# Kernel optimization log

Hardware: AMD Instinct MI355X
Metric: run time of the kernel (lower is better)

The kernel has to match this reference:

```python
import jax, jax.numpy as jnp
import numpy as np

B, D, N, MSRC, H = 4, 256, 2048, 2048, 4
DIM = D // H  # per-head dim = 64
EPS = 1e-3


def _conv1x1(W, b, z):
    # 1x1 Conv1d == per-position linear: W [out,in], z [B,in,N]
    return jnp.einsum('oc,bcn->bon', W, z) + b[None, :, None]


def setup_inputs() -> dict:
    key = jax.random.key(0)
    ks = jax.random.split(key, 20)
    s = 0.05
    x = jax.random.normal(ks[0], (B, D, N), dtype=jnp.float32)
    source = jax.random.normal(ks[1], (B, D, MSRC), dtype=jnp.float32)
    mask = (jax.random.uniform(ks[2], (B, N, MSRC)) > 0.3).astype(jnp.float32)
    Wq = jax.random.normal(ks[3], (D, D), jnp.float32) * s
    bq = jax.random.normal(ks[4], (D,), jnp.float32) * s
    Wk = jax.random.normal(ks[5], (D, D), jnp.float32) * s
    bk = jax.random.normal(ks[6], (D,), jnp.float32) * s
    Wv = jax.random.normal(ks[7], (D, D), jnp.float32) * s
    bv = jax.random.normal(ks[8], (D,), jnp.float32) * s
    Wm = jax.random.normal(ks[9], (D, D), jnp.float32) * s
    bm = jax.random.normal(ks[10], (D,), jnp.float32) * s
    W1 = jax.random.normal(ks[11], (2 * D, 2 * D), jnp.float32) * s
    b1 = jax.random.normal(ks[12], (2 * D,), jnp.float32) * s
    gamma = jnp.ones((2 * D,), jnp.float32)
    beta = jnp.zeros((2 * D,), jnp.float32)
    rmean = jax.random.normal(ks[13], (2 * D,), jnp.float32) * 0.1
    rvar = jax.random.uniform(ks[14], (2 * D,), jnp.float32) + 0.5
    W2 = jax.random.normal(ks[15], (D, 2 * D), jnp.float32) * s
    b2 = jnp.zeros((D,), jnp.float32)  # nn.init.constant_(mlp[-1].bias, 0.0)
    return dict(x=x, source=source, mask=mask, Wq=Wq, bq=bq, Wk=Wk, bk=bk,
                Wv=Wv, bv=bv, Wm=Wm, bm=bm, W1=W1, b1=b1, gamma=gamma,
                beta=beta, rmean=rmean, rvar=rvar, W2=W2, b2=b2)


def reference(x, source, mask, Wq, bq, Wk, bk, Wv, bv, Wm, bm,
              W1, b1, gamma, beta, rmean, rvar, W2, b2):
    b = x.shape[0]
    # channel dim split as (dim, heads) per torch .view(B, dim, H, -1)
    q = _conv1x1(Wq, bq, x).reshape(b, DIM, H, -1)        # [B,d,H,N]
    k = _conv1x1(Wk, bk, source).reshape(b, DIM, H, -1)   # [B,d,H,M]
    v = _conv1x1(Wv, bv, source).reshape(b, DIM, H, -1)   # [B,d,H,M]
    scores = jnp.einsum('bdhn,bdhm->bhnm', q, k) / (DIM ** 0.5)
    neg = -jnp.finfo(scores.dtype).max
    scores = jnp.where(mask[:, None, :, :] > 0, scores, neg)
    prob = jax.nn.softmax(scores, axis=-1)                # [B,H,N,M]
    msg = jnp.einsum('bhnm,bdhm->bdhn', prob, v).reshape(b, D, -1)
    message = _conv1x1(Wm, bm, msg)                       # [B,D,N]
    y = jnp.concatenate([x, message], axis=1)             # [B,2D,N]
    h = _conv1x1(W1, b1, y)
    # BatchNorm1d (eval mode, eps=1e-3)
    h = (h - rmean[None, :, None]) * jax.lax.rsqrt(rvar + EPS)[None, :, None]
    h = h * gamma[None, :, None] + beta[None, :, None]
    h = jax.nn.relu(h)
    return _conv1x1(W2, b2, h)                            # [B,D,N]
```

## Files before the change

### kernel.cpp

```cpp
#include <hip/hip_runtime.h>

constexpr int Bb = 4;
constexpr int Dd = 256;
constexpr int Nn = 2048;
constexpr int Mm = 2048;
constexpr int Hh = 4;
constexpr int D2 = 512;
constexpr int NT = Bb * Nn;

#define FMAXV 3.402823466e38f

typedef _Float16 half8 __attribute__((ext_vector_type(8)));
typedef _Float16 half4v __attribute__((ext_vector_type(4)));
typedef _Float16 half2v __attribute__((ext_vector_type(2)));
typedef float f32x4 __attribute__((ext_vector_type(4)));

typedef const __attribute__((address_space(1))) void* gas_p;
typedef __attribute__((address_space(3))) void* las_p;

__device__ __forceinline__ void gload16(const void* g, void* l) {
    __builtin_amdgcn_global_load_lds((gas_p)g, (las_p)l, 16, 0, 0);
}

__global__ __launch_bounds__(256)
void prep_all_kernel(const float* __restrict__ Wq, const float* __restrict__ bq,
                     const float* __restrict__ Wk, const float* __restrict__ bk,
                     const float* __restrict__ Wv, const float* __restrict__ bv,
                     const float* __restrict__ Wm,
                     const float* __restrict__ W1, const float* __restrict__ b1,
                     const float* __restrict__ gamma, const float* __restrict__ beta,
                     const float* __restrict__ rmean, const float* __restrict__ rvar,
                     const float* __restrict__ W2, const float* __restrict__ mask,
                     const float* __restrict__ x, const float* __restrict__ source,
                     _Float16* __restrict__ Wqp, float* __restrict__ bqp,
                     _Float16* __restrict__ Wkvp, float* __restrict__ bkvp,
                     _Float16* __restrict__ Wmp,
                     _Float16* __restrict__ W1p, float* __restrict__ b1f,
                     _Float16* __restrict__ W2p,
                     unsigned long long* __restrict__ bmask,
                     _Float16* __restrict__ Yp, _Float16* __restrict__ Sp) {
    const int r = blockIdx.x, t = threadIdx.x;
    if (r < 256) {
        const int h = r >> 6, d = r & 63, so = d * Hh + h;
        Wqp[r * 256 + t] = (_Float16)Wq[so * 256 + t];
        if (t == 0) bqp[r] = bq[so];
    } else if (r < 768) {
        const int rr = r - 256, part = rr >> 8, o = rr & 255;
        const int h = o >> 6, d = o & 63, so = d * Hh + h;
        const float* Ws = part ? Wv : Wk;
        const float* bs = part ? bv : bk;
        Wkvp[rr * 256 + t] = (_Float16)Ws[so * 256 + t];
        if (t == 0) bkvp[rr] = bs[so];
    } else if (r < 1024) {
        const int o = r - 768;
        const int h = t >> 6, d = t & 63, sk = d * Hh + h;
        Wmp[o * 256 + t] = (_Float16)Wm[o * 256 + sk];
    } else if (r < 1536) {
        const int o = r - 1024;
        const float s = gamma[o] * rsqrtf(rvar[o] + 1e-3f);
        W1p[o * 512 + t]       = (_Float16)(W1[o * 512 + t] * s);
        W1p[o * 512 + t + 256] = (_Float16)(W1[o * 512 + t + 256] * s);
        if (t == 0) b1f[o] = (b1[o] - rmean[o]) * s + beta[o];
    } else if (r < 1792) {
        const int o = r - 1536;
        W2p[o * 512 + t]       = (_Float16)W2[o * 512 + t];
        W2p[o * 512 + t + 256] = (_Float16)W2[o * 512 + t + 256];
    } else if (r < 3840) {
        const int id = r - 1792;
        const int w = t >> 6, lane = t & 63;
        const int row = id * 4 + w;
        const float* mrow = mask + (size_t)row * Mm;
        unsigned long long* brow = bmask + (size_t)row * (Mm / 64);
        #pragma unroll 4
        for (int word = 0; word < Mm / 64; ++word) {
            const float v = mrow[word * 64 + lane];
            const unsigned long long bits = __ballot(v > 0.f);
            if (lane == 0) brow[word] = bits;
        }
    } else {
        __shared__ _Float16 Ts[64][72];
        const int px = r - 3840;
        const int n0 = (px & 31) * 64, c0 = ((px >> 5) & 3) * 64;
        const int z = px >> 7, b = z >> 1, which = z & 1;
        const float* src = which ? source : x;
        _Float16* dst = which ? Sp : Yp;
        const int stride = which ? 256 : 512;
        const int cl = t >> 2, np = (t & 3) * 16;
        const float* sp = src + ((size_t)b * Dd + c0 + cl) * Nn + n0 + np;
        #pragma unroll
        for (int i = 0; i < 4; ++i) {
            float4 v = *(const float4*)(sp + i * 4);
            Ts[np + i * 4 + 0][cl] = (_Float16)v.x;
            Ts[np + i * 4 + 1][cl] = (_Float16)v.y;
            Ts[np + i * 4 + 2][cl] = (_Float16)v.z;
            Ts[np + i * 4 + 3][cl] = (_Float16)v.w;
        }
        __syncthreads();
        const int nl = t >> 2, cp = (t & 3) * 16;
        half8 a0 = *(const half8*)&Ts[nl][cp];
        half8 a1 = *(const half8*)&Ts[nl][cp + 8];
        _Float16* dp = dst + ((size_t)b * Nn + n0 + nl) * stride + c0 + cp;
        *(half8*)dp = a0;
        *(half8*)(dp + 8) = a1;
    }
}

__global__ __launch_bounds__(256)
void gemm4w_kernel(const _Float16* __restrict__ A, const _Float16* __restrict__ A2,
                   const _Float16* __restrict__ W, const float* __restrict__ bias,
                   _Float16* __restrict__ dst0, _Float16* __restrict__ dst1,
                   _Float16* __restrict__ dst2, float* __restrict__ dstF,
                   int K, int sA, int sOut, int modeSel, int relu, float oscale) {
    __shared__ __align__(16) _Float16 As[2 * 128 * 64];
    __shared__ __align__(16) _Float16 Bs[2 * 64 * 64];

    const int t = threadIdx.x;
    const int w = t >> 6, lane = t & 63, quad = lane >> 4, l16 = lane & 15;
    const int n0 = blockIdx.x * 128;
    const int og0 = blockIdx.y * 64;

    int mode = 0, oloc0 = og0;
    const _Float16* Ab = A;
    int sAl = sA;
    _Float16* d0 = dst0;
    float osc = oscale;
    if (modeSel == 3) {
        const int part = blockIdx.y >> 2;
        if (part == 1)      { Ab = A2; sAl = 256; d0 = dst1; oloc0 = og0 - 256; osc = 1.0f; }
        else if (part == 2) { Ab = A2; sAl = 256; mode = 1; oloc0 = og0 - 512; osc = 1.0f; }
    } else if (modeSel == 2) {
        mode = 2;
    }

    const int srow = t >> 3, sslot = t & 7;
    const int schunk = sslot ^ (srow & 7);

    f32x4 acc[2][4] = {};
    const int nk = K / 64;
    int buf = 0;

    {
        #pragma unroll
        for (int c = 0; c < 4; ++c)
            gload16(Ab + (size_t)(n0 + c * 32 + srow) * sAl + schunk * 8,
                    As + c * 2048 + t * 8);
        #pragma unroll
        for (int c = 0; c < 2; ++c)
            gload16(W + (size_t)(og0 + c * 32 + srow) * K + schunk * 8,
                    Bs + c * 2048 + t * 8);
        __asm__ volatile("s_waitcnt vmcnt(0)" ::: "memory");
        __syncthreads();
    }

    #pragma unroll 1
    for (int kt = 0; kt < nk; ++kt) {
        if (kt + 1 < nk) {
            const int k0 = (kt + 1) * 64, nb = buf ^ 1;
            #pragma unroll
            for (int c = 0; c < 4; ++c)
                gload16(Ab + (size_t)(n0 + c * 32 + srow) * sAl + k0 + schunk * 8,
                        As + nb * 8192 + c * 2048 + t * 8);
            #pragma unroll
            for (int c = 0; c < 2; ++c)
                gload16(W + (size_t)(og0 + c * 32 + srow) * K + k0 + schunk * 8,
                        Bs + nb * 4096 + c * 2048 + t * 8);
        }
        #pragma unroll
        for (int ks = 0; ks < 2; ++ks) {
            const int csw = ((ks * 4 + quad) ^ (l16 & 7)) * 8;
            half8 af[2], bf[4];
            #pragma unroll
            for (int i = 0; i < 2; ++i)
                af[i] = *(const half8*)&As[buf * 8192 + (w * 32 + i * 16 + l16) * 64 + csw];
            #pragma unroll
            for (int j = 0; j < 4; ++j)
                bf[j] = *(const half8*)&Bs[buf * 4096 + (j * 16 + l16) * 64 + csw];
            #pragma unroll
            for (int i = 0; i < 2; ++i)
                #pragma unroll
                for (int j = 0; j < 4; ++j)
                    acc[i][j] = __builtin_amdgcn_mfma_f32_16x16x32_f16(af[i], bf[j], acc[i][j], 0, 0, 0);
        }
        if (kt + 1 < nk) {
            __asm__ volatile("s_waitcnt vmcnt(0)" ::: "memory");
            __syncthreads();
            buf ^= 1;
        }
    }

    float bcol[4];
    #pragma unroll
    for (int j = 0; j < 4; ++j) bcol[j] = bias[og0 + j * 16 + l16];

    if (mode == 0) {
        _Float16* Escr = As + w * 2048;
        #pragma unroll
        for (int i = 0; i < 2; ++i) {
            #pragma unroll
            for (int j = 0; j < 4; ++j)
                #pragma unroll
                for (int reg = 0; reg < 4; ++reg) {
                    float v = (acc[i][j][reg] + bcol[j]) * osc;
                    if (relu) v = fmaxf(v, 0.f);
                    Escr[(quad * 4 + reg) * 72 + j * 16 + l16] = (_Float16)v;
                }
            __asm__ volatile("s_waitcnt lgkmcnt(0)" ::: "memory");
            const int row = lane & 15, oseg = (lane >> 4) * 16;
            half8 e0 = *(const half8*)&Escr[row * 72 + oseg];
            half8 e1 = *(const half8*)&Escr[row * 72 + oseg + 8];
            _Float16* dp = d0 + (size_t)(n0 + w * 32 + i * 16 + row) * sOut + oloc0 + oseg;
            *(half8*)dp = e0;
            *(half8*)(dp + 8) = e1;
            __asm__ volatile("s_waitcnt lgkmcnt(0)" ::: "memory");
        }
    } else if (mode == 1) {
        #pragma unroll
        for (int i = 0; i < 2; ++i)
            #pragma unroll
            for (int j = 0; j < 4; ++j) {
                const int c = j * 16 + l16;
                const int mloc = w * 32 + i * 16 + quad * 4;
                const int sw = l16 * 8;
                half4v pv;
                #pragma unroll
                for (int reg = 0; reg < 4; ++reg)
                    pv[reg] = (_Float16)(acc[i][j][reg] + bcol[j]);
                *(half4v*)&As[c * 128 + (mloc ^ sw)] = pv;
            }
        __syncthreads();
        const int n0m = n0 & 2047, bidx = n0 >> 11;
        #pragma unroll
        for (int r = 0; r < 2; ++r) {
            const int c = (t >> 3) + r * 32;
            const int mch = (t & 7) * 16;
            const int sw = (c & 15) * 8;
            half8 v0 = *(const half8*)&As[c * 128 + (mch ^ sw)];
            half8 v1 = *(const half8*)&As[c * 128 + ((mch + 8) ^ sw)];
            _Float16* dp = dst2 + ((size_t)bidx * 256 + oloc0 + c) * (size_t)Mm + n0m + mch;
            *(half8*)dp = v0;
            *(half8*)(dp + 8) = v1;
        }
    } else {
        __syncthreads();
        float* scr = (float*)As;
        #pragma unroll
        for (int i = 0; i < 2; ++i)
            #pragma unroll
            for (int j = 0; j < 4; ++j) {
                const int c = j * 16 + l16;
                const int mloc = w * 32 + i * 16 + quad * 4;
                const int sw = (c & 7) * 4;
                f32x4 v;
                #pragma unroll
                for (int reg = 0; reg < 4; ++reg) v[reg] = acc[i][j][reg] + bcol[j];
                *(f32x4*)&scr[c * 128 + (mloc ^ sw)] = v;
            }
        __syncthreads();
        const int n0m = n0 & 2047, bidx = n0 >> 11;
        #pragma unroll
        for (int r = 0; r < 2; ++r) {
            const int c = (t >> 3) + r * 32;
            const int mch = (t & 7) * 16;
            const int sw = (c & 7) * 4;
            float* dp = dstF + ((size_t)bidx * 256 + og0 + c) * (size_t)Nn + n0m + mch;
            #pragma unroll
            for (int k = 0; k < 4; ++k)
                *(f32x4*)(dp + k * 4) = *(const f32x4*)&scr[c * 128 + ((mch + k * 4) ^ sw)];
        }
    }
}

__global__ __launch_bounds__(512)
void attn_mfma_kernel(const _Float16* __restrict__ Qp, const _Float16* __restrict__ Kp,
                      const _Float16* __restrict__ Vt,
                      const unsigned int* __restrict__ bmask,
                      _Float16* __restrict__ Oa, _Float16* __restrict__ Ob,
                      _Float16* __restrict__ Oc, _Float16* __restrict__ Od,
                      float* __restrict__ La, float* __restrict__ Lb,
                      float* __restrict__ Lc, float* __restrict__ Ld) {
    __shared__ __align__(16) _Float16 Ks[64][64];
    __shared__ __align__(16) _Float16 Vs[64][64];
    __shared__ __align__(16) _Float16 Ps[8][16][72];

    const int id = blockIdx.x;
    const int xcd = id & 7, loc = id >> 3;
    const int bh = xcd * 2 + (loc >> 6);
    const int sub = loc & 63;
    const int mquart = sub & 3;
    const int n0 = (sub >> 2) * 128;
    const int b = bh >> 2, h = bh & 3;

    const int t = threadIdx.x;
    const int w = t >> 6, lane = t & 63, quad = lane >> 4, l16 = lane & 15;

    const _Float16* qp = Qp + ((size_t)b * Nn + n0 + w * 16 + l16) * 256 + h * 64 + quad * 8;
    const half8 qa0 = *(const half8*)(qp);
    const half8 qa1 = *(const half8*)(qp + 32);

    const _Float16* Kstg = Kp + (size_t)b * Nn * 256 + h * 64;
    const _Float16* Vstg = Vt + ((size_t)b * 256 + h * 64) * (size_t)Mm;
    const int sr = t >> 3;
    const int sl = t & 7;
    const int ss = sl ^ (sr & 7);

    const unsigned int* bmRow = bmask + ((size_t)b * Nn + n0 + w * 16 + l16) * (Mm / 32);

    _Float16* Odst = mquart == 0 ? Oa : mquart == 1 ? Ob : mquart == 2 ? Oc : Od;
    float*    Ldst = mquart == 0 ? La : mquart == 1 ? Lb : mquart == 2 ? Lc : Ld;
    const int mbeg = mquart * (Mm / 4);

    float psum = 0.f;
    f32x4 O[4] = {};

    half8 sk, sv;
    auto stage_load = [&](int m0) {
        sk = *(const half8*)(Kstg + (size_t)(m0 + sr) * 256 + sl * 8);
        sv = *(const half8*)(Vstg + (size_t)sr * Mm + m0 + sl * 8);
    };
    auto stage_write = [&]() {
        *(half8*)&Ks[sr][ss * 8] = sk;
        *(half8*)&Vs[sr][ss * 8] = sv;
    };

    stage_load(mbeg);
    stage_write();
    __syncthreads();

    #pragma unroll 1
    for (int it = 0; it < (Mm / 4) / 64; ++it) {
        const int m0 = mbeg + it * 64;
        if (it < (Mm / 4) / 64 - 1) stage_load(m0 + 64);

        const uint2 bmv = *(const uint2*)(bmRow + (m0 >> 5));

        f32x4 S[4];
        #pragma unroll
        for (int mt = 0; mt < 4; ++mt) {
            const int r = mt * 16 + l16, rs = r & 7;
            half8 k0 = *(const half8*)&Ks[r][(quad ^ rs) * 8];
            half8 k1 = *(const half8*)&Ks[r][((quad + 4) ^ rs) * 8];
            f32x4 z = {0.f, 0.f, 0.f, 0.f};
            z = __builtin_amdgcn_mfma_f32_16x16x32_f16(k0, qa0, z, 0, 0, 0);
            z = __builtin_amdgcn_mfma_f32_16x16x32_f16(k1, qa1, z, 0, 0, 0);
            S[mt] = z;
        }

        const unsigned losh = bmv.x >> (quad * 4);
        const unsigned hish = bmv.y >> (quad * 4);
        #pragma unroll
        for (int mt = 0; mt < 4; ++mt) {
            const unsigned wb = (mt < 2) ? losh : hish;
            const int sh = (mt & 1) * 16;
            const float p0 = ((wb >> (sh + 0)) & 1u) ? __builtin_exp2f(S[mt][0]) : 0.f;
            const float p1 = ((wb >> (sh + 1)) & 1u) ? __builtin_exp2f(S[mt][1]) : 0.f;
            const float p2 = ((wb >> (sh + 2)) & 1u) ? __builtin_exp2f(S[mt][2]) : 0.f;
            const float p3 = ((wb >> (sh + 3)) & 1u) ? __builtin_exp2f(S[mt][3]) : 0.f;
            psum += (p0 + p1) + (p2 + p3);
            const half2v lo2 = __builtin_bit_cast(half2v, __builtin_amdgcn_cvt_pkrtz(p0, p1));
            const half2v hi2 = __builtin_bit_cast(half2v, __builtin_amdgcn_cvt_pkrtz(p2, p3));
            half4v pv;
            pv[0] = lo2[0]; pv[1] = lo2[1]; pv[2] = hi2[0]; pv[3] = hi2[1];
            *(half4v*)&Ps[w][l16][mt * 16 + quad * 4] = pv;
        }
        __asm__ volatile("s_waitcnt lgkmcnt(0)" ::: "memory");
        half8 pa0 = *(const half8*)&Ps[w][l16][quad * 8];
        half8 pa1 = *(const half8*)&Ps[w][l16][32 + quad * 8];

        #pragma unroll
        for (int dt = 0; dt < 4; ++dt) {
            const int r = dt * 16 + l16, rs = r & 7;
            half8 v0 = *(const half8*)&Vs[r][(quad ^ rs) * 8];
            half8 v1 = *(const half8*)&Vs[r][((quad + 4) ^ rs) * 8];
            O[dt] = __builtin_amdgcn_mfma_f32_16x16x32_f16(pa0, v0, O[dt], 0, 0, 0);
            O[dt] = __builtin_amdgcn_mfma_f32_16x16x32_f16(pa1, v1, O[dt], 0, 0, 0);
        }

        if (it < (Mm / 4) / 64 - 1) {
            __syncthreads();
            stage_write();
            __syncthreads();
        }
    }

    psum += __shfl_xor(psum, 16);
    psum += __shfl_xor(psum, 32);

    #pragma unroll
    for (int dt = 0; dt < 4; ++dt)
        #pragma unroll
        for (int reg = 0; reg < 4; ++reg)
            Ps[w][quad * 4 + reg][dt * 16 + l16] = (_Float16)(O[dt][reg] * 0.0625f);
    __asm__ volatile("s_waitcnt lgkmcnt(0)" ::: "memory");
    #pragma unroll
    for (int u2 = 0; u2 < 2; ++u2) {
        const int u = lane * 2 + u2;
        const int r = u >> 3, c = u & 7;
        half8 v = *(const half8*)&Ps[w][r][c * 8];
        *(half8*)(Odst + ((size_t)b * Nn + n0 + w * 16 + r) * 256 + h * 64 + c * 8) = v;
    }
    if (lane < 16)
        Ldst[((size_t)b * Nn + n0 + w * 16 + l16) * 4 + h] = psum * 0.0625f;
}

__global__ __launch_bounds__(256)
void gemm_msg_kernel(const _Float16* __restrict__ Oa, const _Float16* __restrict__ Ob,
                     const _Float16* __restrict__ Oc, const _Float16* __restrict__ Od,
                     const float* __restrict__ La, const float* __restrict__ Lb,
                     const float* __restrict__ Lc, const float* __restrict__ Ld,
                     const _Float16* __restrict__ W, const float* __restrict__ bias,
                     _Float16* __restrict__ dst) {
    __shared__ __align__(16) _Float16 As[2 * 128 * 64];
    __shared__ __align__(16) _Float16 Bs[2 * 64 * 64];

    const int t = threadIdx.x;
    const int w = t >> 6, lane = t & 63, quad = lane >> 4, l16 = lane & 15;
    const int n0 = blockIdx.x * 128;
    const int og0 = blockIdx.y * 64;
    const int srow = t >> 3, sslot = t & 7;
    const int schunk = sslot ^ (srow & 7);
    constexpr int K = 256;

    f32x4 acc[2][4] = {};

    half8 oa[4], ob[4], oc[4], od[4];
    float inv[4];

    auto loadA = [&](int k0) {
        const int h = k0 >> 6;
        #pragma unroll
        for (int c = 0; c < 4; ++c) {
            const size_t row = (size_t)(n0 + c * 32 + srow);
            const size_t off = row * 256 + k0 + schunk * 8;
            oa[c] = *(const half8*)(Oa + off);
            ob[c] = *(const half8*)(Ob + off);
            oc[c] = *(const half8*)(Oc + off);
            od[c] = *(const half8*)(Od + off);
            inv[c] = 1.0f / (La[row * 4 + h] + Lb[row * 4 + h]
                           + Lc[row * 4 + h] + Ld[row * 4 + h]);
        }
    };
    auto writeA = [&](int nb) {
        #pragma unroll
        for (int c = 0; c < 4; ++c) {
            half8 m;
            #pragma unroll
            for (int k = 0; k < 8; ++k)
                m[k] = (_Float16)((((float)oa[c][k] + (float)ob[c][k])
                                 + ((float)oc[c][k] + (float)od[c][k])) * inv[c]);
            *(half8*)&As[nb * 8192 + c * 2048 + t * 8] = m;
        }
    };
    auto loadB = [&](int k0, int nb) {
        #pragma unroll
        for (int c = 0; c < 2; ++c)
            gload16(W + (size_t)(og0 + c * 32 + srow) * K + k0 + schunk * 8,
                    Bs + nb * 4096 + c * 2048 + t * 8);
    };

    loadA(0);
    loadB(0, 0);
    writeA(0);
    __asm__ volatile("s_waitcnt vmcnt(0)" ::: "memory");
    __syncthreads();

    int buf = 0;
    #pragma unroll 1
    for (int kt = 0; kt < 4; ++kt) {
        if (kt < 3) {
            loadA((kt + 1) * 64);
            loadB((kt + 1) * 64, buf ^ 1);
        }
        #pragma unroll
        for (int ks = 0; ks < 2; ++ks) {
            const int csw = ((ks * 4 + quad) ^ (l16 & 7)) * 8;
            half8 af[2], bf[4];
            #pragma unroll
            for (int i = 0; i < 2; ++i)
                af[i] = *(const half8*)&As[buf * 8192 + (w * 32 + i * 16 + l16) * 64 + csw];
            #pragma unroll
            for (int j = 0; j < 4; ++j)
                bf[j] = *(const half8*)&Bs[buf * 4096 + (j * 16 + l16) * 64 + csw];
            #pragma unroll
            for (int i = 0; i < 2; ++i)
                #pragma unroll
                for (int j = 0; j < 4; ++j)
                    acc[i][j] = __builtin_amdgcn_mfma_f32_16x16x32_f16(af[i], bf[j], acc[i][j], 0, 0, 0);
        }
        if (kt < 3) {
            writeA(buf ^ 1);
            __asm__ volatile("s_waitcnt vmcnt(0)" ::: "memory");
            __syncthreads();
            buf ^= 1;
        }
    }

    float bcol[4];
    #pragma unroll
    for (int j = 0; j < 4; ++j) bcol[j] = bias[og0 + j * 16 + l16];

    _Float16* Escr = As + w * 2048;
    #pragma unroll
    for (int i = 0; i < 2; ++i) {
        #pragma unroll
        for (int j = 0; j < 4; ++j)
            #pragma unroll
            for (int reg = 0; reg < 4; ++reg)
                Escr[(quad * 4 + reg) * 72 + j * 16 + l16] =
                    (_Float16)(acc[i][j][reg] + bcol[j]);
        __asm__ volatile("s_waitcnt lgkmcnt(0)" ::: "memory");
        const int row = lane & 15, oseg = (lane >> 4) * 16;
        half8 e0 = *(const half8*)&Escr[row * 72 + oseg];
        half8 e1 = *(const half8*)&Escr[row * 72 + oseg + 8];
        _Float16* dp = dst + (size_t)(n0 + w * 32 + i * 16 + row) * 512 + og0 + oseg;
        *(half8*)dp = e0;
        *(half8*)(dp + 8) = e1;
        __asm__ volatile("s_waitcnt lgkmcnt(0)" ::: "memory");
    }
}

extern "C" void kernel_launch(void* const* d_in, const int* in_sizes, int n_in,
                              void* d_out, int out_size, void* d_ws, size_t ws_size,
                              hipStream_t stream) {
    const float* x      = (const float*)d_in[0];
    const float* source = (const float*)d_in[1];
    const float* mask   = (const float*)d_in[2];
    const float* Wq = (const float*)d_in[3];
    const float* bq = (const float*)d_in[4];
    const float* Wk = (const float*)d_in[5];
    const float* bk = (const float*)d_in[6];
    const float* Wv = (const float*)d_in[7];
    const float* bv = (const float*)d_in[8];
    const float* Wm = (const float*)d_in[9];
    const float* bm = (const float*)d_in[10];
    const float* W1 = (const float*)d_in[11];
    const float* b1 = (const float*)d_in[12];
    const float* gamma = (const float*)d_in[13];
    const float* beta  = (const float*)d_in[14];
    const float* rmean = (const float*)d_in[15];
    const float* rvar  = (const float*)d_in[16];
    const float* W2 = (const float*)d_in[17];
    const float* b2 = (const float*)d_in[18];
    float* outp = (float*)d_out;

    char* wsb = (char*)d_ws;
    _Float16* Yp   = (_Float16*)wsb;
    _Float16* Sp   = (_Float16*)(wsb + (8u << 20));
    _Float16* Qp   = (_Float16*)(wsb + (12u << 20));
    _Float16* Kp   = (_Float16*)(wsb + (16u << 20));
    _Float16* Vt   = (_Float16*)(wsb + (20u << 20));
    _Float16* Oa   = (_Float16*)(wsb + (24u << 20));
    _Float16* Hp   = (_Float16*)(wsb + (28u << 20));
    unsigned long long* bmask = (unsigned long long*)(wsb + (28u << 20));
    _Float16* Ob = (_Float16*)(wsb + (30u << 20));
    float* La = (float*)(wsb + (34u << 20));
    float* Lb = (float*)(wsb + (34u << 20) + (128u << 10));
    float* Lc = (float*)(wsb + (34u << 20) + (256u << 10));
    float* Ld = (float*)(wsb + (34u << 20) + (384u << 10));
    _Float16* Oc = Sp;
    _Float16* Od = (_Float16*)outp;
    char* wp = wsb + (36u << 20);
    _Float16* Wqp  = (_Float16*)wp;            wp += 256 * 256 * 2;
    _Float16* Wkvp = (_Float16*)wp;            wp += 512 * 256 * 2;
    _Float16* Wmp  = (_Float16*)wp;            wp += 256 * 256 * 2;
    _Float16* W1p  = (_Float16*)wp;            wp += 512 * 512 * 2;
    _Float16* W2p  = (_Float16*)wp;            wp += 256 * 512 * 2;
    float* bqp  = (float*)wp;                  wp += 256 * 4;
    float* bkvp = (float*)wp;                  wp += 512 * 4;
    float* b1f  = (float*)wp;                  wp += 512 * 4;

    prep_all_kernel<<<4864, 256, 0, stream>>>(
        Wq, bq, Wk, bk, Wv, bv, Wm, W1, b1, gamma, beta, rmean, rvar, W2, mask,
        x, source, Wqp, bqp, Wkvp, bkvp, Wmp, W1p, b1f, W2p, bmask, Yp, Sp);

    gemm4w_kernel<<<dim3(NT / 128, 12), 256, 0, stream>>>(
        Yp, Sp, Wqp, bqp, Qp, Kp, Vt, nullptr, 256, 512, 256, 3, 0, 0.18033688011f);

    attn_mfma_kernel<<<1024, 512, 0, stream>>>(Qp, Kp, Vt,
                                               (const unsigned int*)bmask,
                                               Oa, Ob, Oc, Od, La, Lb, Lc, Ld);

    gemm_msg_kernel<<<dim3(NT / 128, 4), 256, 0, stream>>>(
        Oa, Ob, Oc, Od, La, Lb, Lc, Ld, Wmp, bm, Yp + 256);

    gemm4w_kernel<<<dim3(NT / 128, 8), 256, 0, stream>>>(
        Yp, nullptr, W1p, b1f, Hp, nullptr, nullptr, nullptr, 512, 512, 512, 0, 1, 1.0f);
    gemm4w_kernel<<<dim3(NT / 128, 4), 256, 0, stream>>>(
        Hp, nullptr, W2p, b2, nullptr, nullptr, nullptr, outp, 512, 512, 0, 2, 0, 1.0f);
}
```

Measured before the change: 237.9 us.

## Double-buffer attention K/V tiles with direct global-to-LDS loads and MFMA priority

The attention kernel's K/V staging now goes through two LDS buffers filled by global_load_lds, so the next tile's load goes straight into the alternate buffer while the current one is computed. This removes the register round-trip and one of the two barriers per iteration. It also raises wave priority around the MFMA sections. The trade-offs are double the K/V LDS footprint, which may lower occupancy, and a vmcnt(0) wait before each barrier.

Measured after the change: 237.8 us. No clear change (-0.0%).

```diff
diff --git a/kernel.cpp b/kernel.cpp
--- a/kernel.cpp
+++ b/kernel.cpp
@@ -278,8 +278,8 @@
                       _Float16* __restrict__ Oc, _Float16* __restrict__ Od,
                       float* __restrict__ La, float* __restrict__ Lb,
                       float* __restrict__ Lc, float* __restrict__ Ld) {
-    __shared__ __align__(16) _Float16 Ks[64][64];
-    __shared__ __align__(16) _Float16 Vs[64][64];
+    __shared__ __align__(16) _Float16 Ks[2][64][64];
+    __shared__ __align__(16) _Float16 Vs[2][64][64];
     __shared__ __align__(16) _Float16 Ps[8][16][72];
 
     const int id = blockIdx.x;
@@ -300,50 +300,50 @@
     const _Float16* Kstg = Kp + (size_t)b * Nn * 256 + h * 64;
     const _Float16* Vstg = Vt + ((size_t)b * 256 + h * 64) * (size_t)Mm;
     const int sr = t >> 3;
-    const int sl = t & 7;
-    const int ss = sl ^ (sr & 7);
+    const int schunk = (t & 7) ^ (sr & 7);
 
     const unsigned int* bmRow = bmask + ((size_t)b * Nn + n0 + w * 16 + l16) * (Mm / 32);
 
     _Float16* Odst = mquart == 0 ? Oa : mquart == 1 ? Ob : mquart == 2 ? Oc : Od;
     float*    Ldst = mquart == 0 ? La : mquart == 1 ? Lb : mquart == 2 ? Lc : Ld;
     const int mbeg = mquart * (Mm / 4);
+    constexpr int NIT = (Mm / 4) / 64;
 
     float psum = 0.f;
     f32x4 O[4] = {};
 
-    half8 sk, sv;
-    auto stage_load = [&](int m0) {
-        sk = *(const half8*)(Kstg + (size_t)(m0 + sr) * 256 + sl * 8);
-        sv = *(const half8*)(Vstg + (size_t)sr * Mm + m0 + sl * 8);
+    auto stage_issue = [&](int m0, int nb) {
+        gload16(Kstg + (size_t)(m0 + sr) * 256 + schunk * 8,
+                (_Float16*)Ks + nb * 4096 + t * 8);
+        gload16(Vstg + (size_t)sr * Mm + m0 + schunk * 8,
+                (_Float16*)Vs + nb * 4096 + t * 8);
     };
-    auto stage_write = [&]() {
-        *(half8*)&Ks[sr][ss * 8] = sk;
-        *(half8*)&Vs[sr][ss * 8] = sv;
-    };
-
-    stage_load(mbeg);
-    stage_write();
+
+    stage_issue(mbeg, 0);
+    __asm__ volatile("s_waitcnt vmcnt(0)" ::: "memory");
     __syncthreads();
 
+    int buf = 0;
     #pragma unroll 1
-    for (int it = 0; it < (Mm / 4) / 64; ++it) {
+    for (int it = 0; it < NIT; ++it) {
         const int m0 = mbeg + it * 64;
-        if (it < (Mm / 4) / 64 - 1) stage_load(m0 + 64);
+        if (it + 1 < NIT) stage_issue(m0 + 64, buf ^ 1);
 
         const uint2 bmv = *(const uint2*)(bmRow + (m0 >> 5));
 
         f32x4 S[4];
+        __builtin_amdgcn_s_setprio(1);
         #pragma unroll
         for (int mt = 0; mt < 4; ++mt) {
             const int r = mt * 16 + l16, rs = r & 7;
-            half8 k0 = *(const half8*)&Ks[r][(quad ^ rs) * 8];
-            half8 k1 = *(const half8*)&Ks[r][((quad + 4) ^ rs) * 8];
+            half8 k0 = *(const half8*)&Ks[buf][r][(quad ^ rs) * 8];
+            half8 k1 = *(const half8*)&Ks[buf][r][((quad + 4) ^ rs) * 8];
             f32x4 z = {0.f, 0.f, 0.f, 0.f};
             z = __builtin_amdgcn_mfma_f32_16x16x32_f16(k0, qa0, z, 0, 0, 0);
             z = __builtin_amdgcn_mfma_f32_16x16x32_f16(k1, qa1, z, 0, 0, 0);
             S[mt] = z;
         }
+        __builtin_amdgcn_s_setprio(0);
 
         const unsigned losh = bmv.x >> (quad * 4);
         const unsigned hish = bmv.y >> (quad * 4);
@@ -366,19 +366,21 @@
         half8 pa0 = *(const half8*)&Ps[w][l16][quad * 8];
         half8 pa1 = *(const half8*)&Ps[w][l16][32 + quad * 8];
 
+        __builtin_amdgcn_s_setprio(1);
         #pragma unroll
         for (int dt = 0; dt < 4; ++dt) {
             const int r = dt * 16 + l16, rs = r & 7;
-            half8 v0 = *(const half8*)&Vs[r][(quad ^ rs) * 8];
-            half8 v1 = *(const half8*)&Vs[r][((quad + 4) ^ rs) * 8];
+            half8 v0 = *(const half8*)&Vs[buf][r][(quad ^ rs) * 8];
+            half8 v1 = *(const half8*)&Vs[buf][r][((quad + 4) ^ rs) * 8];
             O[dt] = __builtin_amdgcn_mfma_f32_16x16x32_f16(pa0, v0, O[dt], 0, 0, 0);
             O[dt] = __builtin_amdgcn_mfma_f32_16x16x32_f16(pa1, v1, O[dt], 0, 0, 0);
         }
-
-        if (it < (Mm / 4) / 64 - 1) {
+        __builtin_amdgcn_s_setprio(0);
+
+        if (it + 1 < NIT) {
+            __asm__ volatile("s_waitcnt vmcnt(0)" ::: "memory");
             __syncthreads();
-            stage_write();
-            __syncthreads();
+            buf ^= 1;
         }
     }
 
```
